# Kernel optimization log

Measured on AMD Instinct MI355X. Metric: run time of the kernel, lower is better.

The kernel has to match this reference:

```python
import jax, jax.numpy as jnp
import numpy as np

B, T, C, FFN, N_LAYER, LAYER_ID = 4, 2048, 1024, 4096, 24, 1
EPS = 1e-5


def setup_inputs() -> dict:
    key = jax.random.key(0)
    ks = jax.random.split(key, 10)
    scale = 0.02

    def w(k, shape):
        return (jax.random.normal(k, shape, jnp.float32) * scale)

    # RWKV-4 init formulas for layer_id=1, n_layer=24 (learned params, init per source)
    r01 = LAYER_ID / (N_LAYER - 1)
    r10 = 1.0 - LAYER_ID / N_LAYER
    ddd = np.arange(C, dtype=np.float64) / C
    h = np.arange(C, dtype=np.float64)
    decay = -5.0 + 8.0 * (h / (C - 1)) ** (0.7 + 1.3 * r01)
    zigzag = np.array([(i + 1) % 3 - 1 for i in range(C)], dtype=np.float64) * 0.5
    tfirst = np.log(0.3) + zigzag

    return {
        "x": jax.random.normal(ks[0], (B, T, C), jnp.float32),
        "ln1_w": jnp.ones((C,), jnp.float32), "ln1_b": jnp.zeros((C,), jnp.float32),
        "ln2_w": jnp.ones((C,), jnp.float32), "ln2_b": jnp.zeros((C,), jnp.float32),
        "time_decay": jnp.asarray(decay, jnp.float32),
        "time_first": jnp.asarray(tfirst, jnp.float32),
        "tmk": jnp.asarray(ddd ** r10, jnp.float32),
        "tmv": jnp.asarray(ddd ** r10 + 0.3 * r01, jnp.float32),
        "tmr": jnp.asarray(ddd ** (0.5 * r10), jnp.float32),
        "att_kw": w(ks[1], (C, C)), "att_vw": w(ks[2], (C, C)),
        "att_rw": w(ks[3], (C, C)), "att_ow": w(ks[4], (C, C)),
        "f_tmk": jnp.asarray(ddd ** r10, jnp.float32),
        "f_tmr": jnp.asarray(ddd ** r10, jnp.float32),
        "f_kw": w(ks[5], (FFN, C)), "f_rw": w(ks[6], (C, C)), "f_vw": w(ks[7], (C, FFN)),
    }


def _ln(z, g, b):
    m = jnp.mean(z, axis=-1, keepdims=True)
    v = jnp.mean(jnp.square(z - m), axis=-1, keepdims=True)
    return (z - m) * jax.lax.rsqrt(v + EPS) * g + b


def _shift(z):  # token shift: prepend zero row along T, drop last
    return jnp.pad(z, ((0, 0), (1, 0), (0, 0)))[:, :-1]


def _wkv(time_decay, u, k, v):
    # Numerically-stable RWKV-4 WKV recurrence (log-space max trick).
    # k, v: [B, T, C]; time_decay, u: [C]
    w = -jnp.exp(time_decay)  # per-channel decay (negative)
    kt = jnp.moveaxis(k, 1, 0)  # [T, B, C]
    vt = jnp.moveaxis(v, 1, 0)
    aa = jnp.zeros_like(kt[0])
    bb = jnp.zeros_like(kt[0])
    pp = jnp.full_like(kt[0], -1e38)

    def step(carry, kv):
        aa, bb, pp = carry
        kk, vv = kv
        ww = u + kk
        p = jnp.maximum(pp, ww)
        e1 = jnp.exp(pp - p)
        e2 = jnp.exp(ww - p)
        out = (e1 * aa + e2 * vv) / (e1 * bb + e2)
        ww2 = pp + w
        p2 = jnp.maximum(ww2, kk)
        e1b = jnp.exp(ww2 - p2)
        e2b = jnp.exp(kk - p2)
        return (e1b * aa + e2b * vv, e1b * bb + e2b, p2), out

    _, out = jax.lax.scan(step, (aa, bb, pp), (kt, vt))
    return jnp.moveaxis(out, 0, 1)  # [B, T, C]


def reference(x, ln1_w, ln1_b, ln2_w, ln2_b, time_decay, time_first,
              tmk, tmv, tmr, att_kw, att_vw, att_rw, att_ow,
              f_tmk, f_tmr, f_kw, f_rw, f_vw):
    # --- RWKV_TimeMix (layer_id != 0; protectors are identity in fwd for finite vals) ---
    h = _ln(x, ln1_w, ln1_b)
    hx = _shift(h)
    xk = h * tmk + hx * (1.0 - tmk)
    xv = h * tmv + hx * (1.0 - tmv)
    xr = h * tmr + hx * (1.0 - tmr)
    k = jnp.einsum('btc,dc->btd', xk, att_kw)
    v = jnp.einsum('btc,dc->btd', xv, att_vw)
    sr = jax.nn.sigmoid(jnp.einsum('btc,dc->btd', xr, att_rw))
    rwkv = sr * _wkv(time_decay, time_first, k, v)
    x = x + jnp.einsum('btd,cd->btc', rwkv, att_ow)
    # --- RWKV_ChannelMix ---
    h = _ln(x, ln2_w, ln2_b)
    hx = _shift(h)
    xk = h * f_tmk + hx * (1.0 - f_tmk)
    xr = h * f_tmr + hx * (1.0 - f_tmr)
    kk = jnp.square(jax.nn.relu(jnp.einsum('btc,fc->btf', xk, f_kw)))
    kv = jnp.einsum('btf,cf->btc', kk, f_vw)
    x = x + jax.nn.sigmoid(jnp.einsum('btc,dc->btd', xr, f_rw)) * kv
    return x
```

## Files before the change

kernel.cpp:

```cpp
#include <hip/hip_runtime.h>
#include <cstdint>

#define C_DIM 1024
#define T_DIM 2048
#define B_DIM 4
#define FFN_DIM 4096
#define NROWS (B_DIM * T_DIM)
#define NELEM ((size_t)NROWS * C_DIM)
#define MB ((size_t)1 << 20)
#define NSEG 32
#define SEGL (T_DIM / NSEG)

typedef __bf16 bf16;
typedef __bf16 bf16x4 __attribute__((ext_vector_type(4)));
typedef __bf16 bf16x8 __attribute__((ext_vector_type(8)));
typedef float  floatx4 __attribute__((ext_vector_type(4)));

#define GLDS(g, l) __builtin_amdgcn_global_load_lds(                          \
    (const __attribute__((address_space(1))) void*)(g),                       \
    (__attribute__((address_space(3))) void*)(l), 16, 0, 0)

__device__ __forceinline__ void store_out(float* p, float v) { *p = v; }
__device__ __forceinline__ void store_out(bf16* p, float v)  { *p = (bf16)v; }

__global__ __launch_bounds__(256) void f2b_kernel(const float* __restrict__ s,
                                                  bf16* __restrict__ d, int n4)
{
    int i = blockIdx.x * 256 + threadIdx.x;
    if (i >= n4) return;
    float4 v = ((const float4*)s)[i];
    bf16x4 o = { (bf16)v.x, (bf16)v.y, (bf16)v.z, (bf16)v.w };
    ((bf16x4*)d)[i] = o;
}

__global__ __launch_bounds__(256) void ln_kernel(const float* __restrict__ x,
                                                 const float* __restrict__ g,
                                                 const float* __restrict__ b,
                                                 float* __restrict__ y)
{
    int row = blockIdx.x;
    int tid = threadIdx.x;
    const float4* xr = (const float4*)(x + (size_t)row * C_DIM);
    float4 v = xr[tid];
    float s  = v.x + v.y + v.z + v.w;
    float s2 = v.x * v.x + v.y * v.y + v.z * v.z + v.w * v.w;
    for (int off = 32; off > 0; off >>= 1) {
        s  += __shfl_down(s,  off);
        s2 += __shfl_down(s2, off);
    }
    __shared__ float red[8];
    int lane = tid & 63, wid = tid >> 6;
    if (lane == 0) { red[wid] = s; red[4 + wid] = s2; }
    __syncthreads();
    s  = red[0] + red[1] + red[2] + red[3];
    s2 = red[4] + red[5] + red[6] + red[7];
    float mean = s * (1.0f / C_DIM);
    float var  = s2 * (1.0f / C_DIM) - mean * mean;
    float inv  = rsqrtf(var + 1e-5f);
    float4 gv = ((const float4*)g)[tid];
    float4 bv = ((const float4*)b)[tid];
    float4 o;
    o.x = (v.x - mean) * inv * gv.x + bv.x;
    o.y = (v.y - mean) * inv * gv.y + bv.y;
    o.z = (v.z - mean) * inv * gv.z + bv.z;
    o.w = (v.w - mean) * inv * gv.w + bv.w;
    ((float4*)(y + (size_t)row * C_DIM))[tid] = o;
}

template<bool HASV>
__global__ __launch_bounds__(256) void mix_kernel(const float* __restrict__ h,
                                                  const float* __restrict__ mk,
                                                  const float* __restrict__ mv,
                                                  const float* __restrict__ mr,
                                                  bf16* __restrict__ xk,
                                                  bf16* __restrict__ xv,
                                                  bf16* __restrict__ xr)
{
    size_t i4 = (size_t)blockIdx.x * 256 + threadIdx.x;
    int c4 = (int)(i4 & (C_DIM / 4 - 1));
    size_t row = i4 >> 8;
    int t = (int)(row & (T_DIM - 1));
    float4 hv = ((const float4*)h)[i4];
    float4 hp = make_float4(0.f, 0.f, 0.f, 0.f);
    if (t != 0) hp = ((const float4*)h)[i4 - C_DIM / 4];

    float4 m1 = ((const float4*)mk)[c4];
    bf16x4 o;
    o.x = (bf16)(hp.x + m1.x * (hv.x - hp.x));
    o.y = (bf16)(hp.y + m1.y * (hv.y - hp.y));
    o.z = (bf16)(hp.z + m1.z * (hv.z - hp.z));
    o.w = (bf16)(hp.w + m1.w * (hv.w - hp.w));
    ((bf16x4*)xk)[i4] = o;

    if (HASV) {
        float4 m2 = ((const float4*)mv)[c4];
        o.x = (bf16)(hp.x + m2.x * (hv.x - hp.x));
        o.y = (bf16)(hp.y + m2.y * (hv.y - hp.y));
        o.z = (bf16)(hp.z + m2.z * (hv.z - hp.z));
        o.w = (bf16)(hp.w + m2.w * (hv.w - hp.w));
        ((bf16x4*)xv)[i4] = o;
    }

    float4 m3 = ((const float4*)mr)[c4];
    o.x = (bf16)(hp.x + m3.x * (hv.x - hp.x));
    o.y = (bf16)(hp.y + m3.y * (hv.y - hp.y));
    o.z = (bf16)(hp.z + m3.z * (hv.z - hp.z));
    o.w = (bf16)(hp.w + m3.w * (hv.w - hp.w));
    ((bf16x4*)xr)[i4] = o;
}

#define EPI_NONE 0
#define EPI_SIG 1
#define EPI_RELU2 2
#define EPI_ADD 3
#define EPI_SCALEADD 4

template<int EPI, typename OutT>
__global__ __launch_bounds__(256) void gemm_bf16(const bf16* __restrict__ A,
                                                 const bf16* __restrict__ W,
                                                 OutT* __restrict__ Y,
                                                 const float* __restrict__ X2,
                                                 const bf16* __restrict__ S,
                                                 int N, int K)
{
    __shared__ unsigned short As[128 * 32];
    __shared__ unsigned short Bs[128 * 32];

    int tid = threadIdx.x;
    int m0 = blockIdx.y * 128, n0 = blockIdx.x * 128;

    const bf16* Ag = A + (size_t)(m0 + (tid >> 2)) * K + (tid & 3) * 8;
    const bf16* Wg = W + (size_t)(n0 + (tid >> 2)) * K + (tid & 3) * 8;
    size_t rowK = (size_t)64 * K;
    int wv = tid >> 6;
    unsigned short* AsW0 = As + wv * 512;
    unsigned short* AsW1 = As + 2048 + wv * 512;
    unsigned short* BsW0 = Bs + wv * 512;
    unsigned short* BsW1 = Bs + 2048 + wv * 512;

    int ln = tid & 63;
    int wm = (wv & 1) * 64, wn = (wv >> 1) * 64;
    int aoff = (wm + (ln & 15)) * 32 + (ln >> 4) * 8;
    int boff = (wn + (ln & 15)) * 32 + (ln >> 4) * 8;

    floatx4 acc[4][4] = {};

    for (int k0 = 0; k0 < K; k0 += 32) {
        if (k0) __syncthreads();
        GLDS(Ag + k0,        AsW0);
        GLDS(Ag + k0 + rowK, AsW1);
        GLDS(Wg + k0,        BsW0);
        GLDS(Wg + k0 + rowK, BsW1);
        __syncthreads();

        bf16x8 a[4], b[4];
#pragma unroll
        for (int i = 0; i < 4; ++i) a[i] = *(const bf16x8*)(As + aoff + i * 512);
#pragma unroll
        for (int j = 0; j < 4; ++j) b[j] = *(const bf16x8*)(Bs + boff + j * 512);
#pragma unroll
        for (int i = 0; i < 4; ++i)
#pragma unroll
            for (int j = 0; j < 4; ++j)
                acc[i][j] = __builtin_amdgcn_mfma_f32_16x16x32_bf16(a[i], b[j], acc[i][j], 0, 0, 0);
    }

    int row0 = (ln >> 4) * 4;
    int colb = n0 + wn + (ln & 15);
#pragma unroll
    for (int i = 0; i < 4; ++i) {
        int gm = m0 + wm + i * 16 + row0;
#pragma unroll
        for (int j = 0; j < 4; ++j) {
            int gn = colb + j * 16;
#pragma unroll
            for (int r = 0; r < 4; ++r) {
                size_t idx = (size_t)(gm + r) * N + gn;
                float v = acc[i][j][r];
                if (EPI == EPI_SIG)        v = 1.0f / (1.0f + __expf(-v));
                else if (EPI == EPI_RELU2) { float t = fmaxf(v, 0.0f); v = t * t; }
                else if (EPI == EPI_ADD)   v = X2[idx] + v;
                else if (EPI == EPI_SCALEADD) v = X2[idx] + (float)S[idx] * v;
                store_out(&Y[idx], v);
            }
        }
    }
}

__global__ __launch_bounds__(256) void wkv_seg(const float* __restrict__ k,
                                               const float* __restrict__ v,
                                               const float* __restrict__ decay,
                                               float* __restrict__ sa,
                                               float* __restrict__ sb,
                                               float* __restrict__ sp)
{
    int idx = blockIdx.x * 256 + threadIdx.x;
    int c   = idx & (C_DIM - 1);
    int bs  = idx >> 10;
    int seg = bs & (NSEG - 1);
    int b   = bs >> 5;
    float w = -__expf(decay[c]);
    size_t base = ((size_t)b * T_DIM + (size_t)seg * SEGL) * C_DIM + c;
    float aa = 0.f, bb = 0.f, pp = -1e38f;
    for (int t = 0; t < SEGL; ++t) {
        size_t off = base + (size_t)t * C_DIM;
        float kk = k[off], vv = v[off];
        float ww2 = pp + w;
        float p2  = fmaxf(ww2, kk);
        float e1  = __expf(ww2 - p2);
        float e2  = __expf(kk - p2);
        aa = e1 * aa + e2 * vv;
        bb = e1 * bb + e2;
        pp = p2;
    }
    sa[idx] = aa; sb[idx] = bb; sp[idx] = pp;
}

__global__ __launch_bounds__(256) void wkv_comb(const float* __restrict__ sa,
                                                const float* __restrict__ sb,
                                                const float* __restrict__ sp,
                                                const float* __restrict__ decay,
                                                float* __restrict__ ia,
                                                float* __restrict__ ib,
                                                float* __restrict__ ip)
{
    int idx = blockIdx.x * 256 + threadIdx.x;
    int c = idx & (C_DIM - 1);
    int b = idx >> 10;
    float wL = -__expf(decay[c]) * (float)SEGL;
    float aa = 0.f, bb = 0.f, pp = -1e38f;
    size_t base = (size_t)b * NSEG * C_DIM + c;
    for (int j = 0; j < NSEG; ++j) {
        size_t o = base + (size_t)j * C_DIM;
        ia[o] = aa; ib[o] = bb; ip[o] = pp;
        float a_s = sa[o], b_s = sb[o], p_s = sp[o];
        float pd = pp + wL;
        float pn = fmaxf(pd, p_s);
        float e1 = __expf(pd - pn);
        float e2 = __expf(p_s - pn);
        aa = e1 * aa + e2 * a_s;
        bb = e1 * bb + e2 * b_s;
        pp = pn;
    }
}

__global__ __launch_bounds__(256) void wkv_out(const float* __restrict__ k,
                                               const float* __restrict__ v,
                                               const float* __restrict__ sr,
                                               const float* __restrict__ decay,
                                               const float* __restrict__ first,
                                               const float* __restrict__ ia,
                                               const float* __restrict__ ib,
                                               const float* __restrict__ ip,
                                               bf16* __restrict__ out)
{
    int idx = blockIdx.x * 256 + threadIdx.x;
    int c   = idx & (C_DIM - 1);
    int bs  = idx >> 10;
    int seg = bs & (NSEG - 1);
    int b   = bs >> 5;
    float w = -__expf(decay[c]);
    float u = first[c];
    float aa = ia[idx], bb = ib[idx], pp = ip[idx];
    size_t base = ((size_t)b * T_DIM + (size_t)seg * SEGL) * C_DIM + c;
    for (int t = 0; t < SEGL; ++t) {
        size_t off = base + (size_t)t * C_DIM;
        float kk = k[off], vv = v[off];
        float ww = u + kk;
        float p  = fmaxf(pp, ww);
        float e1 = __expf(pp - p);
        float e2 = __expf(ww - p);
        float o  = (e1 * aa + e2 * vv) / (e1 * bb + e2);
        out[off] = (bf16)(sr[off] * o);
        float ww2 = pp + w;
        float p2  = fmaxf(ww2, kk);
        float e1b = __expf(ww2 - p2);
        float e2b = __expf(kk - p2);
        aa = e1b * aa + e2b * vv;
        bb = e1b * bb + e2b;
        pp = p2;
    }
}

extern "C" void kernel_launch(void* const* d_in, const int* in_sizes, int n_in,
                              void* d_out, int out_size, void* d_ws, size_t ws_size,
                              hipStream_t stream)
{
    const float* x          = (const float*)d_in[0];
    const float* ln1_w      = (const float*)d_in[1];
    const float* ln1_b      = (const float*)d_in[2];
    const float* ln2_w      = (const float*)d_in[3];
    const float* ln2_b      = (const float*)d_in[4];
    const float* time_decay = (const float*)d_in[5];
    const float* time_first = (const float*)d_in[6];
    const float* tmk        = (const float*)d_in[7];
    const float* tmv        = (const float*)d_in[8];
    const float* tmr        = (const float*)d_in[9];
    const float* att_kw     = (const float*)d_in[10];
    const float* att_vw     = (const float*)d_in[11];
    const float* att_rw     = (const float*)d_in[12];
    const float* att_ow     = (const float*)d_in[13];
    const float* f_tmk      = (const float*)d_in[14];
    const float* f_tmr      = (const float*)d_in[15];
    const float* f_kw       = (const float*)d_in[16];
    const float* f_rw       = (const float*)d_in[17];
    const float* f_vw       = (const float*)d_in[18];
    float* out = (float*)d_out;

    char* W8 = (char*)d_ws;
    bf16* kw_b  = (bf16*)(W8 + 0 * MB);
    bf16* vw_b  = (bf16*)(W8 + 2 * MB);
    bf16* rw_b  = (bf16*)(W8 + 4 * MB);
    bf16* ow_b  = (bf16*)(W8 + 6 * MB);
    bf16* fkw_b = (bf16*)(W8 + 8 * MB);
    bf16* frw_b = (bf16*)(W8 + 16 * MB);
    bf16* fvw_b = (bf16*)(W8 + 18 * MB);

    bf16*  xk_b   = (bf16*)(W8 + 26 * MB);
    bf16*  xv_b   = (bf16*)(W8 + 42 * MB);
    bf16*  xr_b   = (bf16*)(W8 + 58 * MB);
    bf16*  rwkv_b = xk_b;
    bf16*  xk2_b  = (bf16*)(W8 + 26 * MB);
    bf16*  xr2_b  = (bf16*)(W8 + 42 * MB);
    bf16*  sr2_b  = (bf16*)(W8 + 58 * MB);
    float* h      = (float*)(W8 + 74 * MB);
    float* kbuf   = (float*)(W8 + 74 * MB);
    float* vbuf   = (float*)(W8 + 106 * MB);
    float* srb    = (float*)(W8 + 138 * MB);
    float* h2     = (float*)(W8 + 74 * MB);
    bf16*  kk_b   = (bf16*)(W8 + 106 * MB);

    size_t KB512 = (size_t)512 * 1024;
    float* sc_a = (float*)(W8 + 170 * MB);
    float* sc_b = (float*)(W8 + 170 * MB + 1 * KB512);
    float* sc_p = (float*)(W8 + 170 * MB + 2 * KB512);
    float* in_a = (float*)(W8 + 170 * MB + 3 * KB512);
    float* in_b = (float*)(W8 + 170 * MB + 4 * KB512);
    float* in_p = (float*)(W8 + 170 * MB + 5 * KB512);

    int nC = C_DIM * C_DIM / 4, nF = FFN_DIM * C_DIM / 4;
    f2b_kernel<<<(nC + 255) / 256, 256, 0, stream>>>(att_kw, kw_b, nC);
    f2b_kernel<<<(nC + 255) / 256, 256, 0, stream>>>(att_vw, vw_b, nC);
    f2b_kernel<<<(nC + 255) / 256, 256, 0, stream>>>(att_rw, rw_b, nC);
    f2b_kernel<<<(nC + 255) / 256, 256, 0, stream>>>(att_ow, ow_b, nC);
    f2b_kernel<<<(nF + 255) / 256, 256, 0, stream>>>(f_kw, fkw_b, nF);
    f2b_kernel<<<(nC + 255) / 256, 256, 0, stream>>>(f_rw, frw_b, nC);
    f2b_kernel<<<(nF + 255) / 256, 256, 0, stream>>>(f_vw, fvw_b, nF);

    int mixGrid = (int)(NELEM / 4 / 256);
    dim3 gC(C_DIM / 128, NROWS / 128);
    dim3 gF(FFN_DIM / 128, NROWS / 128);
    int segGrid = B_DIM * NSEG * C_DIM / 256;

    ln_kernel<<<NROWS, 256, 0, stream>>>(x, ln1_w, ln1_b, h);
    mix_kernel<true><<<mixGrid, 256, 0, stream>>>(h, tmk, tmv, tmr, xk_b, xv_b, xr_b);
    gemm_bf16<EPI_NONE, float><<<gC, 256, 0, stream>>>(xk_b, kw_b, kbuf, nullptr, nullptr, C_DIM, C_DIM);
    gemm_bf16<EPI_NONE, float><<<gC, 256, 0, stream>>>(xv_b, vw_b, vbuf, nullptr, nullptr, C_DIM, C_DIM);
    gemm_bf16<EPI_SIG,  float><<<gC, 256, 0, stream>>>(xr_b, rw_b, srb,  nullptr, nullptr, C_DIM, C_DIM);
    wkv_seg<<<segGrid, 256, 0, stream>>>(kbuf, vbuf, time_decay, sc_a, sc_b, sc_p);
    wkv_comb<<<B_DIM * C_DIM / 256, 256, 0, stream>>>(sc_a, sc_b, sc_p, time_decay, in_a, in_b, in_p);
    wkv_out<<<segGrid, 256, 0, stream>>>(kbuf, vbuf, srb, time_decay, time_first,
                                         in_a, in_b, in_p, rwkv_b);
    gemm_bf16<EPI_ADD,  float><<<gC, 256, 0, stream>>>(rwkv_b, ow_b, out, x, nullptr, C_DIM, C_DIM);

    ln_kernel<<<NROWS, 256, 0, stream>>>(out, ln2_w, ln2_b, h2);
    mix_kernel<false><<<mixGrid, 256, 0, stream>>>(h2, f_tmk, nullptr, f_tmr, xk2_b, nullptr, xr2_b);
    gemm_bf16<EPI_SIG,   bf16><<<gC, 256, 0, stream>>>(xr2_b, frw_b, sr2_b, nullptr, nullptr, C_DIM, C_DIM);
    gemm_bf16<EPI_RELU2, bf16><<<gF, 256, 0, stream>>>(xk2_b, fkw_b, kk_b, nullptr, nullptr, FFN_DIM, C_DIM);
    gemm_bf16<EPI_SCALEADD, float><<<gC, 256, 0, stream>>>(kk_b, fvw_b, out, out, sr2_b, C_DIM, FFN_DIM);
}
```

Baseline: 599.6 us.

## Fuse LN with token-shift mix, batch weight casts, swizzle GEMM LDS and tiles

LayerNorm and the token-shift mix are merged into one kernel that recomputes the previous row's statistics, so the fp32 normalized buffer is never written or reread. The seven weight-conversion launches become a single launch. The GEMM gains an XOR-style LDS swizzle against bank conflicts and a 1D grid with a remapped tile order aimed at better L2 reuse. The receptance sigmoid output is stored as bf16 instead of fp32, halving that traffic at a small precision cost.

```diff
diff --git a/kernel.cpp b/kernel.cpp
--- a/kernel.cpp
+++ b/kernel.cpp
@@ -23,68 +23,85 @@
 __device__ __forceinline__ void store_out(float* p, float v) { *p = v; }
 __device__ __forceinline__ void store_out(bf16* p, float v)  { *p = (bf16)v; }
 
-__global__ __launch_bounds__(256) void f2b_kernel(const float* __restrict__ s,
-                                                  bf16* __restrict__ d, int n4)
-{
-    int i = blockIdx.x * 256 + threadIdx.x;
-    if (i >= n4) return;
-    float4 v = ((const float4*)s)[i];
+struct W7 {
+    const float* s[7];
+    bf16*        d[7];
+    int          cum[8];
+};
+
+__global__ __launch_bounds__(256) void f2b7_kernel(W7 w)
+{
+    int id = blockIdx.x * 256 + threadIdx.x;
+    int seg = 0;
+#pragma unroll
+    for (int j = 1; j < 7; ++j) if (id >= w.cum[j]) seg = j;
+    int i = id - w.cum[seg];
+    float4 v = ((const float4*)w.s[seg])[i];
     bf16x4 o = { (bf16)v.x, (bf16)v.y, (bf16)v.z, (bf16)v.w };
-    ((bf16x4*)d)[i] = o;
-}
-
-__global__ __launch_bounds__(256) void ln_kernel(const float* __restrict__ x,
-                                                 const float* __restrict__ g,
-                                                 const float* __restrict__ b,
-                                                 float* __restrict__ y)
+    ((bf16x4*)w.d[seg])[i] = o;
+}
+
+template<bool HASV>
+__global__ __launch_bounds__(256) void lnmix_kernel(const float* __restrict__ x,
+                                                    const float* __restrict__ g,
+                                                    const float* __restrict__ b,
+                                                    const float* __restrict__ mk,
+                                                    const float* __restrict__ mv,
+                                                    const float* __restrict__ mr,
+                                                    bf16* __restrict__ xk,
+                                                    bf16* __restrict__ xv,
+                                                    bf16* __restrict__ xr)
 {
     int row = blockIdx.x;
+    int t   = row & (T_DIM - 1);
     int tid = threadIdx.x;
-    const float4* xr = (const float4*)(x + (size_t)row * C_DIM);
-    float4 v = xr[tid];
-    float s  = v.x + v.y + v.z + v.w;
-    float s2 = v.x * v.x + v.y * v.y + v.z * v.z + v.w * v.w;
+    size_t i4 = (size_t)row * 256 + tid;
+
+    float4 v  = ((const float4*)x)[i4];
+    float4 vp = make_float4(0.f, 0.f, 0.f, 0.f);
+    if (t != 0) vp = ((const float4*)x)[i4 - 256];
+
+    float s   = v.x + v.y + v.z + v.w;
+    float s2  = v.x * v.x + v.y * v.y + v.z * v.z + v.w * v.w;
+    float sp  = vp.x + vp.y + vp.z + vp.w;
+    float sp2 = vp.x * vp.x + vp.y * vp.y + vp.z * vp.z + vp.w * vp.w;
     for (int off = 32; off > 0; off >>= 1) {
-        s  += __shfl_down(s,  off);
-        s2 += __shfl_down(s2, off);
-    }
-    __shared__ float red[8];
+        s   += __shfl_down(s,   off);
+        s2  += __shfl_down(s2,  off);
+        sp  += __shfl_down(sp,  off);
+        sp2 += __shfl_down(sp2, off);
+    }
+    __shared__ float red[16];
     int lane = tid & 63, wid = tid >> 6;
-    if (lane == 0) { red[wid] = s; red[4 + wid] = s2; }
+    if (lane == 0) { red[wid] = s; red[4 + wid] = s2; red[8 + wid] = sp; red[12 + wid] = sp2; }
     __syncthreads();
-    s  = red[0] + red[1] + red[2] + red[3];
-    s2 = red[4] + red[5] + red[6] + red[7];
-    float mean = s * (1.0f / C_DIM);
-    float var  = s2 * (1.0f / C_DIM) - mean * mean;
-    float inv  = rsqrtf(var + 1e-5f);
+    s   = red[0] + red[1] + red[2] + red[3];
+    s2  = red[4] + red[5] + red[6] + red[7];
+    sp  = red[8] + red[9] + red[10] + red[11];
+    sp2 = red[12] + red[13] + red[14] + red[15];
+
+    float mean  = s * (1.0f / C_DIM);
+    float inv   = rsqrtf(s2 * (1.0f / C_DIM) - mean * mean + 1e-5f);
+    float meanp = sp * (1.0f / C_DIM);
+    float invp  = rsqrtf(sp2 * (1.0f / C_DIM) - meanp * meanp + 1e-5f);
+
     float4 gv = ((const float4*)g)[tid];
     float4 bv = ((const float4*)b)[tid];
-    float4 o;
-    o.x = (v.x - mean) * inv * gv.x + bv.x;
-    o.y = (v.y - mean) * inv * gv.y + bv.y;
-    o.z = (v.z - mean) * inv * gv.z + bv.z;
-    o.w = (v.w - mean) * inv * gv.w + bv.w;
-    ((float4*)(y + (size_t)row * C_DIM))[tid] = o;
-}
-
-template<bool HASV>
-__global__ __launch_bounds__(256) void mix_kernel(const float* __restrict__ h,
-                                                  const float* __restrict__ mk,
-                                                  const float* __restrict__ mv,
-                                                  const float* __restrict__ mr,
-                                                  bf16* __restrict__ xk,
-                                                  bf16* __restrict__ xv,
-                                                  bf16* __restrict__ xr)
-{
-    size_t i4 = (size_t)blockIdx.x * 256 + threadIdx.x;
-    int c4 = (int)(i4 & (C_DIM / 4 - 1));
-    size_t row = i4 >> 8;
-    int t = (int)(row & (T_DIM - 1));
-    float4 hv = ((const float4*)h)[i4];
-    float4 hp = make_float4(0.f, 0.f, 0.f, 0.f);
-    if (t != 0) hp = ((const float4*)h)[i4 - C_DIM / 4];
-
-    float4 m1 = ((const float4*)mk)[c4];
+    float4 hv, hp;
+    hv.x = (v.x - mean) * inv * gv.x + bv.x;
+    hv.y = (v.y - mean) * inv * gv.y + bv.y;
+    hv.z = (v.z - mean) * inv * gv.z + bv.z;
+    hv.w = (v.w - mean) * inv * gv.w + bv.w;
+    if (t != 0) {
+        hp.x = (vp.x - meanp) * invp * gv.x + bv.x;
+        hp.y = (vp.y - meanp) * invp * gv.y + bv.y;
+        hp.z = (vp.z - meanp) * invp * gv.z + bv.z;
+        hp.w = (vp.w - meanp) * invp * gv.w + bv.w;
+    } else {
+        hp = make_float4(0.f, 0.f, 0.f, 0.f);
+    }
+
+    float4 m1 = ((const float4*)mk)[tid];
     bf16x4 o;
     o.x = (bf16)(hp.x + m1.x * (hv.x - hp.x));
     o.y = (bf16)(hp.y + m1.y * (hv.y - hp.y));
@@ -93,7 +110,7 @@
     ((bf16x4*)xk)[i4] = o;
 
     if (HASV) {
-        float4 m2 = ((const float4*)mv)[c4];
+        float4 m2 = ((const float4*)mv)[tid];
         o.x = (bf16)(hp.x + m2.x * (hv.x - hp.x));
         o.y = (bf16)(hp.y + m2.y * (hv.y - hp.y));
         o.z = (bf16)(hp.z + m2.z * (hv.z - hp.z));
@@ -101,7 +118,7 @@
         ((bf16x4*)xv)[i4] = o;
     }
 
-    float4 m3 = ((const float4*)mr)[c4];
+    float4 m3 = ((const float4*)mr)[tid];
     o.x = (bf16)(hp.x + m3.x * (hv.x - hp.x));
     o.y = (bf16)(hp.y + m3.y * (hv.y - hp.y));
     o.z = (bf16)(hp.z + m3.z * (hv.z - hp.z));
@@ -127,10 +144,18 @@
     __shared__ unsigned short Bs[128 * 32];
 
     int tid = threadIdx.x;
-    int m0 = blockIdx.y * 128, n0 = blockIdx.x * 128;
-
-    const bf16* Ag = A + (size_t)(m0 + (tid >> 2)) * K + (tid & 3) * 8;
-    const bf16* Wg = W + (size_t)(n0 + (tid >> 2)) * K + (tid & 3) * 8;
+    int ntn    = N >> 7;
+    int stride = ntn >> 3;
+    int id  = blockIdx.x;
+    int sq  = id >> 3;
+    int n_t = (id & 7) * stride + (sq % stride);
+    int m_t = sq / stride;
+    int m0 = m_t * 128, n0 = n_t * 128;
+
+    int r0  = tid >> 2;
+    int qsw = ((tid & 3) - ((r0 >> 1) & 3)) & 3;
+    const bf16* Ag = A + (size_t)(m0 + r0) * K + qsw * 8;
+    const bf16* Wg = W + (size_t)(n0 + r0) * K + qsw * 8;
     size_t rowK = (size_t)64 * K;
     int wv = tid >> 6;
     unsigned short* AsW0 = As + wv * 512;
@@ -140,8 +165,11 @@
 
     int ln = tid & 63;
     int wm = (wv & 1) * 64, wn = (wv >> 1) * 64;
-    int aoff = (wm + (ln & 15)) * 32 + (ln >> 4) * 8;
-    int boff = (wn + (ln & 15)) * 32 + (ln >> 4) * 8;
+    int ra0 = wm + (ln & 15);
+    int rb0 = wn + (ln & 15);
+    int qa  = ln >> 4;
+    int abase = ra0 * 32 + (((qa + (ra0 >> 1)) & 3) * 8);
+    int bbase = rb0 * 32 + (((qa + (rb0 >> 1)) & 3) * 8);
 
     floatx4 acc[4][4] = {};
 
@@ -155,9 +183,9 @@
 
         bf16x8 a[4], b[4];
 #pragma unroll
-        for (int i = 0; i < 4; ++i) a[i] = *(const bf16x8*)(As + aoff + i * 512);
-#pragma unroll
-        for (int j = 0; j < 4; ++j) b[j] = *(const bf16x8*)(Bs + boff + j * 512);
+        for (int i = 0; i < 4; ++i) a[i] = *(const bf16x8*)(As + abase + i * 512);
+#pragma unroll
+        for (int j = 0; j < 4; ++j) b[j] = *(const bf16x8*)(Bs + bbase + j * 512);
 #pragma unroll
         for (int i = 0; i < 4; ++i)
 #pragma unroll
@@ -246,7 +274,7 @@
 
 __global__ __launch_bounds__(256) void wkv_out(const float* __restrict__ k,
                                                const float* __restrict__ v,
-                                               const float* __restrict__ sr,
+                                               const bf16* __restrict__ sr,
                                                const float* __restrict__ decay,
                                                const float* __restrict__ first,
                                                const float* __restrict__ ia,
@@ -271,7 +299,7 @@
         float e1 = __expf(pp - p);
         float e2 = __expf(ww - p);
         float o  = (e1 * aa + e2 * vv) / (e1 * bb + e2);
-        out[off] = (bf16)(sr[off] * o);
+        out[off] = (bf16)((float)sr[off] * o);
         float ww2 = pp + w;
         float p2  = fmaxf(ww2, kk);
         float e1b = __expf(ww2 - p2);
@@ -323,11 +351,9 @@
     bf16*  xk2_b  = (bf16*)(W8 + 26 * MB);
     bf16*  xr2_b  = (bf16*)(W8 + 42 * MB);
     bf16*  sr2_b  = (bf16*)(W8 + 58 * MB);
-    float* h      = (float*)(W8 + 74 * MB);
     float* kbuf   = (float*)(W8 + 74 * MB);
     float* vbuf   = (float*)(W8 + 106 * MB);
-    float* srb    = (float*)(W8 + 138 * MB);
-    float* h2     = (float*)(W8 + 74 * MB);
+    bf16*  srb_b  = (bf16*)(W8 + 138 * MB);
     bf16*  kk_b   = (bf16*)(W8 + 106 * MB);
 
     size_t KB512 = (size_t)512 * 1024;
@@ -338,33 +364,33 @@
     float* in_b = (float*)(W8 + 170 * MB + 4 * KB512);
     float* in_p = (float*)(W8 + 170 * MB + 5 * KB512);
 
-    int nC = C_DIM * C_DIM / 4, nF = FFN_DIM * C_DIM / 4;
-    f2b_kernel<<<(nC + 255) / 256, 256, 0, stream>>>(att_kw, kw_b, nC);
-    f2b_kernel<<<(nC + 255) / 256, 256, 0, stream>>>(att_vw, vw_b, nC);
-    f2b_kernel<<<(nC + 255) / 256, 256, 0, stream>>>(att_rw, rw_b, nC);
-    f2b_kernel<<<(nC + 255) / 256, 256, 0, stream>>>(att_ow, ow_b, nC);
-    f2b_kernel<<<(nF + 255) / 256, 256, 0, stream>>>(f_kw, fkw_b, nF);
-    f2b_kernel<<<(nC + 255) / 256, 256, 0, stream>>>(f_rw, frw_b, nC);
-    f2b_kernel<<<(nF + 255) / 256, 256, 0, stream>>>(f_vw, fvw_b, nF);
-
-    int mixGrid = (int)(NELEM / 4 / 256);
-    dim3 gC(C_DIM / 128, NROWS / 128);
-    dim3 gF(FFN_DIM / 128, NROWS / 128);
+    int nC4 = C_DIM * C_DIM / 4, nF4 = FFN_DIM * C_DIM / 4;
+    W7 w7;
+    const float* srcs[7] = { att_kw, att_vw, att_rw, att_ow, f_kw, f_rw, f_vw };
+    bf16*        dsts[7] = { kw_b, vw_b, rw_b, ow_b, fkw_b, frw_b, fvw_b };
+    int          cnts[7] = { nC4, nC4, nC4, nC4, nF4, nC4, nF4 };
+    int cum = 0;
+    for (int i = 0; i < 7; ++i) { w7.s[i] = srcs[i]; w7.d[i] = dsts[i]; w7.cum[i] = cum; cum += cnts[i]; }
+    w7.cum[7] = cum;
+    f2b7_kernel<<<cum / 256, 256, 0, stream>>>(w7);
+
+    dim3 gC(8 * 64);
+    dim3 gF(32 * 64);
     int segGrid = B_DIM * NSEG * C_DIM / 256;
 
-    ln_kernel<<<NROWS, 256, 0, stream>>>(x, ln1_w, ln1_b, h);
-    mix_kernel<true><<<mixGrid, 256, 0, stream>>>(h, tmk, tmv, tmr, xk_b, xv_b, xr_b);
+    lnmix_kernel<true><<<NROWS, 256, 0, stream>>>(x, ln1_w, ln1_b, tmk, tmv, tmr,
+                                                  xk_b, xv_b, xr_b);
     gemm_bf16<EPI_NONE, float><<<gC, 256, 0, stream>>>(xk_b, kw_b, kbuf, nullptr, nullptr, C_DIM, C_DIM);
     gemm_bf16<EPI_NONE, float><<<gC, 256, 0, stream>>>(xv_b, vw_b, vbuf, nullptr, nullptr, C_DIM, C_DIM);
-    gemm_bf16<EPI_SIG,  float><<<gC, 256, 0, stream>>>(xr_b, rw_b, srb,  nullptr, nullptr, C_DIM, C_DIM);
+    gemm_bf16<EPI_SIG,  bf16 ><<<gC, 256, 0, stream>>>(xr_b, rw_b, srb_b, nullptr, nullptr, C_DIM, C_DIM);
     wkv_seg<<<segGrid, 256, 0, stream>>>(kbuf, vbuf, time_decay, sc_a, sc_b, sc_p);
     wkv_comb<<<B_DIM * C_DIM / 256, 256, 0, stream>>>(sc_a, sc_b, sc_p, time_decay, in_a, in_b, in_p);
-    wkv_out<<<segGrid, 256, 0, stream>>>(kbuf, vbuf, srb, time_decay, time_first,
+    wkv_out<<<segGrid, 256, 0, stream>>>(kbuf, vbuf, srb_b, time_decay, time_first,
                                          in_a, in_b, in_p, rwkv_b);
     gemm_bf16<EPI_ADD,  float><<<gC, 256, 0, stream>>>(rwkv_b, ow_b, out, x, nullptr, C_DIM, C_DIM);
 
-    ln_kernel<<<NROWS, 256, 0, stream>>>(out, ln2_w, ln2_b, h2);
-    mix_kernel<false><<<mixGrid, 256, 0, stream>>>(h2, f_tmk, nullptr, f_tmr, xk2_b, nullptr, xr2_b);
+    lnmix_kernel<false><<<NROWS, 256, 0, stream>>>(out, ln2_w, ln2_b, f_tmk, nullptr, f_tmr,
+                                                   xk2_b, nullptr, xr2_b);
     gemm_bf16<EPI_SIG,   bf16><<<gC, 256, 0, stream>>>(xr2_b, frw_b, sr2_b, nullptr, nullptr, C_DIM, C_DIM);
     gemm_bf16<EPI_RELU2, bf16><<<gF, 256, 0, stream>>>(xk2_b, fkw_b, kk_b, nullptr, nullptr, FFN_DIM, C_DIM);
     gemm_bf16<EPI_SCALEADD, float><<<gC, 256, 0, stream>>>(kk_b, fvw_b, out, out, sr2_b, C_DIM, FFN_DIM);
```

Measured after the change: 562.4 us. -6.2%, faster.
